# Kernel optimization log

Hardware: AMD Instinct MI355X
Metric: run time of the kernel (lower is better)

## Reference

```python
import jax, jax.numpy as jnp
import numpy as np
from jax import lax

B, C, L = 64, 768, 197
DEG = 3          # KACN Chebyshev degree
KW = 3           # conv kernel size
EPS = 1e-5       # BatchNorm eps
END_X = 14.0     # RoPE grid width (14x14 patch grid + 1 CLS token)


def _conv1d(x, W):
    # x: (B, Cin, L), W: (Cout, Cin, K); padding=1 keeps length
    return lax.conv_general_dilated(x, W, window_strides=(1,), padding=[(1, 1)],
                                    dimension_numbers=('NCH', 'OIH', 'NCH'))


def _batchnorm(y, scale, bias):
    # training-mode BatchNorm1d: biased stats over (batch, length)
    mean = jnp.mean(y, axis=(0, 2), keepdims=True)
    var = jnp.var(y, axis=(0, 2), keepdims=True)
    return (y - mean) * lax.rsqrt(var + EPS) * scale[None, :, None] + bias[None, :, None]


def _kacn_proj(x, W, scale, bias):
    # KACNConv1DLayer (groups=1): cos(arange(deg+1) * arccos(tanh(x))) basis, conv, BN
    b, c, l = x.shape
    z = jnp.arccos(jnp.tanh(x))[:, :, None, :] * jnp.arange(DEG + 1, dtype=x.dtype)[None, None, :, None]
    z = jnp.cos(z).reshape(b, c * (DEG + 1), l)  # (B, C*(DEG+1), L), channel-major pairing
    return _batchnorm(_conv1d(z, W), scale, bias)


def _rope(t, cosang, sinang):
    # rotate consecutive channel pairs; t: (B, N, C), cos/sin: (N, C//2)
    b, n, c = t.shape
    p = t.reshape(b, n, c // 2, 2)
    a, bb = p[..., 0], p[..., 1]
    ra = a * cosang[None] - bb * sinang[None]
    rb = a * sinang[None] + bb * cosang[None]
    return jnp.stack([ra, rb], axis=-1).reshape(b, n, c)


def reference(x, Wq, Wk, Wv, bnq_s, bnq_b, bnk_s, bnk_b, bnv_s, bnv_b, gamma, freqs, norm_s, norm_b):
    q = _kacn_proj(x, Wq, bnq_s, bnq_b)
    k = _kacn_proj(x, Wk, bnk_s, bnk_b)
    v = _kacn_proj(x, Wv, bnv_s, bnv_b)
    b, c, l = v.shape
    Q = q.transpose(0, 2, 1)  # (B, L, C)
    K = k.transpose(0, 2, 1)
    # mixed 2D RoPE angles (num_heads=1): t_x, t_y over 14x14 grid
    t = jnp.arange(l - 1, dtype=x.dtype)
    tx = jnp.mod(t, END_X)
    ty = jnp.floor(t / END_X)
    ang = tx[:, None] * freqs[0][None, :] + ty[:, None] * freqs[1][None, :]  # (L-1, C//2)
    cosang, sinang = jnp.cos(ang), jnp.sin(ang)
    # token 0 (CLS) is not rotated
    Qr = jnp.concatenate([Q[:, :1], _rope(Q[:, 1:], cosang, sinang)], axis=1)
    Kr = jnp.concatenate([K[:, :1], _rope(K[:, 1:], cosang, sinang)], axis=1)
    energy = jnp.einsum('bic,bjc->bij', Qr, Kr)          # unscaled, as in the module
    att = jax.nn.softmax(energy, axis=-1)
    out = jnp.einsum('bcj,bij->bci', v, att)             # v @ att^T
    return _batchnorm(gamma[0] * x + out, norm_s, norm_b)


def setup_inputs() -> dict:
    key = jax.random.key(0)
    ks = jax.random.split(key, 5)
    std = 1.0 / (C * (DEG + 1) * KW)
    x = jax.random.normal(ks[0], (B, C, L), dtype=jnp.float32)
    Wq = jax.random.normal(ks[1], (C, C * (DEG + 1), KW), dtype=jnp.float32) * std
    Wk = jax.random.normal(ks[2], (C, C * (DEG + 1), KW), dtype=jnp.float32) * std
    Wv = jax.random.normal(ks[3], (C, C * (DEG + 1), KW), dtype=jnp.float32) * std
    ones = jnp.ones((C,), jnp.float32)
    zeros = jnp.zeros((C,), jnp.float32)
    # init_2d_freqs(dim=C, num_heads=1, theta=10, rotate=True).view(2, -1)
    mag = 1.0 / 10.0 ** (np.arange(0, C, 4)[: C // 4].astype(np.float32) / C)
    ang = float(jax.random.uniform(ks[4], ())) * 2.0 * np.pi
    fx = np.concatenate([mag * np.cos(ang), mag * np.cos(np.pi / 2 + ang)])
    fy = np.concatenate([mag * np.sin(ang), mag * np.sin(np.pi / 2 + ang)])
    freqs = jnp.asarray(np.stack([fx, fy], axis=0), dtype=jnp.float32)  # (2, C//2)
    return {"x": x, "Wq": Wq, "Wk": Wk, "Wv": Wv,
            "bnq_s": ones, "bnq_b": zeros, "bnk_s": ones, "bnk_b": zeros,
            "bnv_s": ones, "bnv_b": zeros,
            "gamma": jnp.zeros((1,), jnp.float32), "freqs": freqs,
            "norm_s": ones, "norm_b": zeros}
```

## Files before the change

### kernel.cpp

```cpp
#include <hip/hip_runtime.h>

#define CCH 768
#define LL  197
#define L199 199
#define KC  2304
#define KTOT 6912
#define MK2 1769472
#define NVALID 12736
#define NROW 12608

typedef __bf16 bf16x8 __attribute__((ext_vector_type(8)));
typedef float f32x4 __attribute__((ext_vector_type(4)));
typedef float f32x16 __attribute__((ext_vector_type(16)));

__device__ __forceinline__ unsigned short f2bf(float f) {
  unsigned int u = __float_as_uint(f);
  u += 0x7FFFu + ((u >> 16) & 1u);
  return (unsigned short)(u >> 16);
}
__device__ __forceinline__ float bf2f(unsigned short h) {
  return __uint_as_float(((unsigned int)h) << 16);
}

__global__ void bias_k(const float* __restrict__ Wq, const float* __restrict__ Wk,
                       const float* __restrict__ Wv, float* __restrict__ bias3) {
  int u = blockIdx.x * 256 + threadIdx.x;
  if (u >= 9 * 768) return;
  int proj = u / 2304, rem = u % 2304, tap = rem / 768, m = rem % 768;
  const float* W = proj == 0 ? Wq : (proj == 1 ? Wk : Wv);
  float s = 0.f;
  for (int c = 0; c < 768; ++c) s += W[((size_t)m * 3072 + c * 4) * 3 + tap];
  bias3[u] = s;
}

__global__ void pack_w3(const float* __restrict__ Wq, const float* __restrict__ Wk,
                        const float* __restrict__ Wv, unsigned short* __restrict__ Apack,
                        size_t pack1_halves) {
  int u = blockIdx.x * 256 + threadIdx.x;
  if (u >= MK2) return;
  int proj = blockIdx.y;
  const float* W = proj == 0 ? Wq : (proj == 1 ? Wk : Wv);
  unsigned short* Ahi = Apack + (size_t)proj * pack1_halves;
  unsigned short* Alo = Ahi + (size_t)768 * KTOT;
  int m = u / KC, kc = u % KC;
  int c = kc / 3, dm1 = kc % 3;
  int ci = c * 4 + dm1 + 1;
  const float* src = W + ((size_t)m * 3072 + ci) * 3;
#pragma unroll
  for (int tap = 0; tap < 3; ++tap) {
    float f = src[tap];
    unsigned short hi = f2bf(f);
    unsigned short lo = f2bf(f - bf2f(hi));
    size_t idx = (size_t)m * KTOT + tap * KC + kc;
    Ahi[idx] = hi;
    Alo[idx] = lo;
  }
}

__global__ void z_kernel(const float* __restrict__ x, unsigned short* __restrict__ Zhi,
                         unsigned short* __restrict__ Zlo) {
  __shared__ float zs[3][32][33];
  int c0 = blockIdx.x * 32, l0 = blockIdx.y * 32, b = blockIdx.z;
  int t = threadIdx.x;
#pragma unroll
  for (int s = 0; s < 4; ++s) {
    int u = t + 256 * s;
    int rc = u >> 5, cl = u & 31;
    float v = 0.f;
    if (l0 + cl < LL) v = x[((size_t)b * CCH + c0 + rc) * LL + l0 + cl];
    float t1 = tanhf(v);
    zs[0][rc][cl] = t1;
    zs[1][rc][cl] = 2.f * t1 * t1 - 1.f;
    zs[2][rc][cl] = t1 * (4.f * t1 * t1 - 3.f);
  }
  __syncthreads();
#pragma unroll
  for (int s = 0; s < 12; ++s) {
    int w = t + 256 * s;
    int rl = w / 96, cc = w % 96;
    if (l0 + rl < LL) {
      int cl2 = cc / 3, dm1 = cc % 3;
      float v = zs[dm1][cl2][rl];
      unsigned short hi = f2bf(v);
      unsigned short lo = f2bf(v - bf2f(hi));
      size_t row = (size_t)b * L199 + 1 + l0 + rl;
      Zhi[row * KC + c0 * 3 + cc] = hi;
      Zlo[row * KC + c0 * 3 + cc] = lo;
    }
  }
}

__global__ void zero_zpad(unsigned short* __restrict__ Zhi, unsigned short* __restrict__ Zlo) {
  int u = blockIdx.x * 256 + threadIdx.x;
  if (u >= 132 * KC) return;
  int rowi = u / KC, c = u % KC;
  size_t r = (rowi < 128) ? ((size_t)(rowi >> 1) * L199 + (size_t)(rowi & 1) * 198)
                          : ((size_t)NVALID + rowi - 128);
  Zhi[r * KC + c] = 0;
  Zlo[r * KC + c] = 0;
}

#define GLL(SRC, DST) \
  __builtin_amdgcn_global_load_lds( \
      (const __attribute__((address_space(1))) void*)(SRC), \
      (__attribute__((address_space(3))) void*)(DST), 16, 0, 0)

__global__ __launch_bounds__(512, 2) void conv_gemm3(const unsigned short* __restrict__ Apack,
                                                     const unsigned short* __restrict__ Zhi,
                                                     const unsigned short* __restrict__ Zlo,
                                                     const float* __restrict__ bias3,
                                                     float* __restrict__ Oqk,
                                                     float* __restrict__ Ov) {
  __shared__ unsigned short lds[2 * 4 * 8192];
  const int bid = blockIdx.x;
  const int xcd = bid & 7, loc = bid >> 3;
  const int wg = (xcd < 2) ? (xcd * 57 + loc) : (114 + (xcd - 2) * 56 + loc);
  const int n_t = wg / 9, rem = wg % 9;
  const int proj = rem / 3, m_t = rem % 3;
  const int m_blk = m_t * 256, n_blk = n_t * 256;
  const unsigned short* Ahi = Apack + (size_t)proj * 2 * 768 * KTOT;
  const unsigned short* Alo = Ahi + (size_t)768 * KTOT;
  const float* bias3p = bias3 + proj * 2304;
  float* Op = (proj == 2) ? Ov : Oqk + (size_t)proj * NROW * CCH;

  const int t = threadIdx.x;
  const int wave = t >> 6, lane = t & 63;
  const int wm = (wave >> 2) * 128, wn = (wave & 3) * 64;
  f32x16 acc[4][2] = {};

  const int lt = ((lane >> 4) & 1) * 512 + (lane >> 5) * 128 + (lane & 15) * 8;
  const int auoff = (wm >> 4) * 512 + lt;
  const int buoff = (wn >> 4) * 512 + lt;

  const int prow = lane & 15;
  const int kch = lane >> 4;
  const unsigned short* srcs[8];
  int doff[8];
#pragma unroll
  for (int j = 0; j < 8; ++j) {
    int u = (wave << 3) + j;
    int tile = u >> 4, p = u & 15;
    doff[j] = tile * 8192 + p * 512;
    int r;
    const unsigned short* g;
    int rs;
    if (tile < 2) {
      r = m_blk + p * 16 + prow;
      g = (tile == 0) ? Ahi : Alo;
      rs = KTOT;
    } else {
      r = n_blk + p * 16 + prow;
      if (r > 12737) r = 12737;
      g = (tile == 2) ? Zhi : Zlo;
      rs = KC;
    }
    srcs[j] = g + (size_t)r * rs + kch * 8;
  }

  const int NIT = KTOT / 32;
#pragma unroll
  for (int j = 0; j < 8; ++j) GLL(srcs[j], lds + doff[j]);
#pragma unroll
  for (int j = 0; j < 6; ++j) GLL(srcs[j] + 32, lds + 32768 + doff[j]);
  asm volatile("s_waitcnt vmcnt(6)\n\ts_barrier" ::: "memory");
  __builtin_amdgcn_sched_barrier(0);

  for (int i = 0; i < NIT; ++i) {
    const unsigned short* lb = lds + ((i & 1) ? 32768 : 0);
    unsigned short* othbuf = lds + ((i & 1) ? 0 : 32768);
    unsigned short* curbuf = lds + ((i & 1) ? 32768 : 0);
    const int koff_prev = 32 * (i + 1);
    const int koff_cur  = 32 * (i + 2);
    const bool stage_prev = (i < NIT - 1);
    const bool stage_cur  = (i < NIT - 2);

    bf16x8 bh[2][2], bl[2][2];
    bf16x8 ah[2], al[2];

#pragma unroll
    for (int ks = 0; ks < 2; ++ks) {
#pragma unroll
      for (int nb = 0; nb < 2; ++nb) {
        bh[nb][ks] = *(const bf16x8*)(lb + 16384 + buoff + nb * 1024 + ks * 256);
        bl[nb][ks] = *(const bf16x8*)(lb + 24576 + buoff + nb * 1024 + ks * 256);
      }
      ah[ks] = *(const bf16x8*)(lb + auoff + ks * 256);
      al[ks] = *(const bf16x8*)(lb + 8192 + auoff + ks * 256);
    }
    if (stage_prev) {
      GLL(srcs[6] + koff_prev, othbuf + doff[6]);
      GLL(srcs[7] + koff_prev, othbuf + doff[7]);
    }
    asm volatile("s_barrier\n\ts_waitcnt lgkmcnt(0)" ::: "memory");
    __builtin_amdgcn_sched_barrier(0);
    __builtin_amdgcn_s_setprio(1);
#pragma unroll
    for (int p = 0; p < 3; ++p)
#pragma unroll
      for (int ks = 0; ks < 2; ++ks)
#pragma unroll
        for (int nb = 0; nb < 2; ++nb) {
          acc[0][nb] = __builtin_amdgcn_mfma_f32_32x32x16_bf16(
              p == 2 ? al[ks] : ah[ks], p == 1 ? bl[nb][ks] : bh[nb][ks], acc[0][nb], 0, 0, 0);
        }
    __builtin_amdgcn_s_setprio(0);
    asm volatile("s_barrier" ::: "memory");
    __builtin_amdgcn_sched_barrier(0);

#define PHASEQ(Q)                                                                 \
    {                                                                             \
      _Pragma("unroll") for (int ks = 0; ks < 2; ++ks) {                          \
        ah[ks] = *(const bf16x8*)(lb + auoff + (Q) * 1024 + ks * 256);            \
        al[ks] = *(const bf16x8*)(lb + 8192 + auoff + (Q) * 1024 + ks * 256);     \
      }                                                                           \
      if (stage_cur) {                                                            \
        GLL(srcs[2 * ((Q) - 1)] + koff_cur, curbuf + doff[2 * ((Q) - 1)]);        \
        GLL(srcs[2 * ((Q) - 1) + 1] + koff_cur, curbuf + doff[2 * ((Q) - 1) + 1]);\
      }                                                                           \
      asm volatile("s_barrier\n\ts_waitcnt lgkmcnt(0)" ::: "memory");             \
      __builtin_amdgcn_sched_barrier(0);                                          \
      __builtin_amdgcn_s_setprio(1);                                              \
      _Pragma("unroll") for (int p = 0; p < 3; ++p)                               \
      _Pragma("unroll") for (int ks = 0; ks < 2; ++ks)                            \
      _Pragma("unroll") for (int nb = 0; nb < 2; ++nb) {                          \
        acc[Q][nb] = __builtin_amdgcn_mfma_f32_32x32x16_bf16(                     \
            p == 2 ? al[ks] : ah[ks], p == 1 ? bl[nb][ks] : bh[nb][ks],           \
            acc[Q][nb], 0, 0, 0);                                                 \
      }                                                                           \
      __builtin_amdgcn_s_setprio(0);                                              \
    }

    PHASEQ(1)
    asm volatile("s_barrier" ::: "memory");
    __builtin_amdgcn_sched_barrier(0);
    PHASEQ(2)
    asm volatile("s_barrier" ::: "memory");
    __builtin_amdgcn_sched_barrier(0);
    PHASEQ(3)
    if (i < NIT - 2) {
      asm volatile("s_waitcnt vmcnt(6)\n\ts_barrier" ::: "memory");
    } else if (i == NIT - 2) {
      asm volatile("s_waitcnt vmcnt(0)\n\ts_barrier" ::: "memory");
    }
    __builtin_amdgcn_sched_barrier(0);
#undef PHASEQ
  }

  int rowarr[2];
  bool val[2], v0[2], v2[2];
#pragma unroll
  for (int nb = 0; nb < 2; ++nb) {
    int n = n_blk + wn + nb * 32 + (lane & 31);
    int b = n / L199, nl = n - b * L199;
    val[nb] = (n < NVALID) && (nl < LL);
    rowarr[nb] = b * LL + nl;
    v0[nb] = (nl == 0);
    v2[nb] = (nl == 196);
  }
#pragma unroll
  for (int mb = 0; mb < 4; ++mb) {
#pragma unroll
    for (int q = 0; q < 4; ++q) {
      int m = m_blk + wm + mb * 32 + q * 8 + (lane >> 5) * 4;
      f32x4 b0 = *(const f32x4*)(bias3p + m);
      f32x4 b1 = *(const f32x4*)(bias3p + 768 + m);
      f32x4 b2 = *(const f32x4*)(bias3p + 1536 + m);
      f32x4 bs = b0 + b1 + b2;
#pragma unroll
      for (int nb = 0; nb < 2; ++nb) {
        if (val[nb]) {
          f32x4 r;
          r[0] = acc[mb][nb][q * 4 + 0];
          r[1] = acc[mb][nb][q * 4 + 1];
          r[2] = acc[mb][nb][q * 4 + 2];
          r[3] = acc[mb][nb][q * 4 + 3];
          r += bs;
          if (v0[nb]) r -= b0;
          if (v2[nb]) r -= b2;
          *(f32x4*)(Op + (size_t)rowarr[nb] * CCH + m) = r;
        }
      }
    }
  }
}

__global__ void zero_f32(float* __restrict__ p, int n) {
  int u = blockIdx.x * 256 + threadIdx.x;
  if (u < n) p[u] = 0.f;
}

__global__ void bn_stats(const float* __restrict__ Oqk, const float* __restrict__ Ov,
                         float* __restrict__ Ssum, float* __restrict__ Ssq) {
  int proj = blockIdx.z;
  int cb = blockIdx.x * 64;
  int rb = blockIdx.y;
  int t = threadIdx.x;
  int ch = cb + (t & 63);
  int phase = t >> 6;
  const float* Op = (proj == 2) ? Ov : Oqk + (size_t)proj * NROW * CCH;
  float s = 0.f, q = 0.f;
  for (int r = rb * 394 + phase; r < rb * 394 + 394; r += 4) {
    float v = Op[(size_t)r * CCH + ch];
    s += v; q += v * v;
  }
  __shared__ float rs[256], rq[256];
  rs[t] = s; rq[t] = q;
  __syncthreads();
  if (t < 64) {
    float S = rs[t] + rs[t + 64] + rs[t + 128] + rs[t + 192];
    float Q = rq[t] + rq[t + 64] + rq[t + 128] + rq[t + 192];
    atomicAdd(&Ssum[proj * CCH + cb + t], S);
    atomicAdd(&Ssq[proj * CCH + cb + t], Q);
  }
}

__global__ void bn_fin(const float* __restrict__ Ssum, const float* __restrict__ Ssq,
                       const float* __restrict__ sq, const float* __restrict__ bq,
                       const float* __restrict__ sk, const float* __restrict__ bk,
                       const float* __restrict__ sv, const float* __restrict__ bv,
                       float* __restrict__ abn) {
  int u = blockIdx.x * 256 + threadIdx.x;
  if (u >= 3 * CCH) return;
  int proj = u / CCH, ch = u % CCH;
  float mean = Ssum[u] / 12608.f;
  float var = Ssq[u] / 12608.f - mean * mean;
  const float* sc = proj == 0 ? sq : (proj == 1 ? sk : sv);
  const float* bi = proj == 0 ? bq : (proj == 1 ? bk : bv);
  float a = sc[ch] * rsqrtf(var + 1e-5f);
  abn[u * 2] = a;
  abn[u * 2 + 1] = bi[ch] - mean * a;
}

__global__ void rope_pack(const float* __restrict__ Oqk, const float* __restrict__ abn,
                          const float* __restrict__ freqs, float* __restrict__ Qr,
                          float* __restrict__ Kr) {
  size_t u = (size_t)blockIdx.x * 256 + threadIdx.x;
  if (u >= 64ull * LL * 384) return;
  int c2 = (int)(u % 384);
  int l = (int)((u / 384) % LL);
  int b = (int)(u / (384ull * LL));
  size_t rowO = ((size_t)b * LL + l) * CCH + 2 * c2;
  const float* Ok = Oqk + (size_t)NROW * CCH;
  float q0 = Oqk[rowO], q1 = Oqk[rowO + 1];
  float k0 = Ok[rowO], k1 = Ok[rowO + 1];
  float aq0 = abn[(2 * c2) * 2],                bq0 = abn[(2 * c2) * 2 + 1];
  float aq1 = abn[(2 * c2 + 1) * 2],            bq1 = abn[(2 * c2 + 1) * 2 + 1];
  float ak0 = abn[(CCH + 2 * c2) * 2],          bk0 = abn[(CCH + 2 * c2) * 2 + 1];
  float ak1 = abn[(CCH + 2 * c2 + 1) * 2],      bk1 = abn[(CCH + 2 * c2 + 1) * 2 + 1];
  q0 = q0 * aq0 + bq0; q1 = q1 * aq1 + bq1;
  k0 = k0 * ak0 + bk0; k1 = k1 * ak1 + bk1;
  if (l > 0) {
    int tt = l - 1;
    float tx = (float)(tt % 14), ty = (float)(tt / 14);
    float ang = tx * freqs[c2] + ty * freqs[384 + c2];
    float sn, cs;
    sincosf(ang, &sn, &cs);
    float r0 = q0 * cs - q1 * sn, r1 = q0 * sn + q1 * cs;
    q0 = r0; q1 = r1;
    r0 = k0 * cs - k1 * sn; r1 = k0 * sn + k1 * cs;
    k0 = r0; k1 = r1;
  }
  size_t rowT = ((size_t)b * LL + l) * CCH + 2 * c2;
  Qr[rowT] = q0; Qr[rowT + 1] = q1;
  Kr[rowT] = k0; Kr[rowT + 1] = k1;
}

__global__ void energy_k(const float* __restrict__ Qr, const float* __restrict__ Kr,
                         float* __restrict__ E) {
  __shared__ float Qs[32][33], Ks[32][33];
  int i0 = blockIdx.x * 32, j0 = blockIdx.y * 32, b = blockIdx.z;
  int t = threadIdx.x, tj = t & 31, ti = t >> 5;
  float acc[4] = {0.f, 0.f, 0.f, 0.f};
  const float* Qb = Qr + (size_t)b * LL * CCH;
  const float* Kb = Kr + (size_t)b * LL * CCH;
  for (int k0 = 0; k0 < CCH; k0 += 32) {
    __syncthreads();
#pragma unroll
    for (int s = 0; s < 4; ++s) {
      int u = t + 256 * s, r = u >> 5, cc = u & 31;
      Qs[r][cc] = (i0 + r < LL) ? Qb[(size_t)(i0 + r) * CCH + k0 + cc] : 0.f;
      Ks[r][cc] = (j0 + r < LL) ? Kb[(size_t)(j0 + r) * CCH + k0 + cc] : 0.f;
    }
    __syncthreads();
#pragma unroll
    for (int kk = 0; kk < 32; ++kk) {
      float kv = Ks[tj][kk];
#pragma unroll
      for (int q = 0; q < 4; ++q) acc[q] += Qs[ti * 4 + q][kk] * kv;
    }
  }
#pragma unroll
  for (int q = 0; q < 4; ++q) {
    int i = i0 + ti * 4 + q, j = j0 + tj;
    if (i < LL && j < LL) E[((size_t)b * LL + i) * LL + j] = acc[q];
  }
}

__global__ void softmax_k(float* __restrict__ E) {
  int row = blockIdx.x;
  int lane = threadIdx.x;
  float* Er = E + (size_t)row * LL;
  float v[4];
  float m = -3.4e38f;
#pragma unroll
  for (int q = 0; q < 4; ++q) {
    int j = lane + 64 * q;
    v[q] = (j < LL) ? Er[j] : -3.4e38f;
    m = fmaxf(m, v[q]);
  }
  for (int off = 32; off; off >>= 1) m = fmaxf(m, __shfl_down(m, off));
  m = __shfl(m, 0);
  float s = 0.f;
#pragma unroll
  for (int q = 0; q < 4; ++q) {
    int j = lane + 64 * q;
    v[q] = (j < LL) ? expf(v[q] - m) : 0.f;
    s += v[q];
  }
  for (int off = 32; off; off >>= 1) s += __shfl_down(s, off);
  s = __shfl(s, 0);
  float inv = 1.f / s;
#pragma unroll
  for (int q = 0; q < 4; ++q) {
    int j = lane + 64 * q;
    if (j < LL) Er[j] = v[q] * inv;
  }
}

__global__ void av_k(const float* __restrict__ att, const float* __restrict__ Ov,
                     const float* __restrict__ abn, float* __restrict__ OA) {
  __shared__ float As[32][33];
  __shared__ float Vs[32][64];
  int i0 = blockIdx.x * 32, c0 = blockIdx.y * 64, b = blockIdx.z;
  int t = threadIdx.x, tc = t & 63, tq = t >> 6;
  const float* attb = att + (size_t)b * LL * LL;
  float acc[8] = {};
  for (int j0 = 0; j0 < LL; j0 += 32) {
    __syncthreads();
#pragma unroll
    for (int s = 0; s < 4; ++s) {
      int u = t + 256 * s, r = u >> 5, cc = u & 31;
      As[r][cc] = (i0 + r < LL && j0 + cc < LL) ? attb[(size_t)(i0 + r) * LL + j0 + cc] : 0.f;
    }
#pragma unroll
    for (int s = 0; s < 8; ++s) {
      int u = t + 256 * s, r = u >> 6, cc = u & 63;
      Vs[r][cc] = (j0 + r < LL) ? Ov[((size_t)b * LL + j0 + r) * CCH + c0 + cc] : 0.f;
    }
    __syncthreads();
#pragma unroll
    for (int jj = 0; jj < 32; ++jj) {
      float vv = Vs[jj][tc];
#pragma unroll
      for (int q = 0; q < 8; ++q) acc[q] += As[tq * 8 + q][jj] * vv;
    }
  }
  float a = abn[(2 * CCH + c0 + tc) * 2], bb = abn[(2 * CCH + c0 + tc) * 2 + 1];
#pragma unroll
  for (int q = 0; q < 8; ++q) {
    int i = i0 + tq * 8 + q;
    if (i < LL) OA[((size_t)b * LL + i) * CCH + c0 + tc] = a * acc[q] + bb;
  }
}

__global__ void trans_y(const float* __restrict__ OA, const float* __restrict__ x,
                        const float* __restrict__ gamma, float* __restrict__ Y) {
  __shared__ float Ts[32][33];
  int l0 = blockIdx.x * 32, c0 = blockIdx.y * 32, b = blockIdx.z;
  int t = threadIdx.x;
  float g = gamma[0];
#pragma unroll
  for (int s = 0; s < 4; ++s) {
    int u = t + 256 * s, r = u >> 5, cc = u & 31;
    Ts[r][cc] = (l0 + r < LL) ? OA[((size_t)b * LL + l0 + r) * CCH + c0 + cc] : 0.f;
  }
  __syncthreads();
#pragma unroll
  for (int s = 0; s < 4; ++s) {
    int u = t + 256 * s, rc = u >> 5, cl = u & 31;
    if (l0 + cl < LL) {
      size_t idx = ((size_t)b * CCH + c0 + rc) * LL + l0 + cl;
      Y[idx] = g * x[idx] + Ts[cl][rc];
    }
  }
}

__global__ void bn_y(const float* __restrict__ Y, const float* __restrict__ ns,
                     const float* __restrict__ nb, float* __restrict__ fab) {
  int c = blockIdx.x;
  int t = threadIdx.x;
  float s = 0.f, q = 0.f;
  for (int u = t; u < 12608; u += 256) {
    int b = u / LL, l = u % LL;
    float v = Y[((size_t)b * CCH + c) * LL + l];
    s += v; q += v * v;
  }
  __shared__ float rs[256], rq[256];
  rs[t] = s; rq[t] = q;
  __syncthreads();
  for (int off = 128; off; off >>= 1) {
    if (t < off) { rs[t] += rs[t + off]; rq[t] += rq[t + off]; }
    __syncthreads();
  }
  if (t == 0) {
    float mean = rs[0] / 12608.f, var = rq[0] / 12608.f - mean * mean;
    float a = ns[c] * rsqrtf(var + 1e-5f);
    fab[c * 2] = a;
    fab[c * 2 + 1] = nb[c] - mean * a;
  }
}

__global__ void final_k(const float* __restrict__ Y, const float* __restrict__ fab,
                        float* __restrict__ out) {
  size_t u = (size_t)blockIdx.x * 256 + threadIdx.x;
  if (u >= 64ull * CCH * LL) return;
  int c = (int)((u / LL) % CCH);
  out[u] = fab[c * 2] * Y[u] + fab[c * 2 + 1];
}

extern "C" void kernel_launch(void* const* d_in, const int* in_sizes, int n_in,
                              void* d_out, int out_size, void* d_ws, size_t ws_size,
                              hipStream_t stream) {
  const float* x = (const float*)d_in[0];
  const float* Wq = (const float*)d_in[1];
  const float* Wk = (const float*)d_in[2];
  const float* Wv = (const float*)d_in[3];
  const float* bnq_s = (const float*)d_in[4];
  const float* bnq_b = (const float*)d_in[5];
  const float* bnk_s = (const float*)d_in[6];
  const float* bnk_b = (const float*)d_in[7];
  const float* bnv_s = (const float*)d_in[8];
  const float* bnv_b = (const float*)d_in[9];
  const float* gamma = (const float*)d_in[10];
  const float* freqs = (const float*)d_in[11];
  const float* norm_s = (const float*)d_in[12];
  const float* norm_b = (const float*)d_in[13];
  float* out = (float*)d_out;

  char* ws = (char*)d_ws;
  const size_t QRSZ  = 38731776;
  const size_t PACK1 = 21233664;
  const size_t ZSZ   = 58705920;

  const size_t OFS_PACK = 0;
  const size_t OFS_Z    = 3 * PACK1;
  const size_t OFS_ZLO  = OFS_Z + ZSZ;
  const size_t OFS_O    = OFS_ZLO + ZSZ;
  const size_t OFS_MISC = OFS_O + 2 * QRSZ;

  unsigned short* Apack = (unsigned short*)(ws + OFS_PACK);
  unsigned short* Zhi = (unsigned short*)(ws + OFS_Z);
  unsigned short* Zlo = (unsigned short*)(ws + OFS_ZLO);
  float* Oqk = (float*)(ws + OFS_O);
  float* bias3 = (float*)(ws + OFS_MISC);
  float* Ssum = (float*)(ws + OFS_MISC + 27648);
  float* Ssq  = (float*)(ws + OFS_MISC + 36864);
  float* abn  = (float*)(ws + OFS_MISC + 46080);
  float* fab  = (float*)(ws + OFS_MISC + 64512);
  float* Ov = out;
  float* Qr = (float*)(ws + OFS_Z);
  float* Kr = (float*)(ws + OFS_Z + QRSZ);
  float* E  = (float*)(ws + OFS_Z + 2 * QRSZ);
  float* OA = (float*)(ws + OFS_Z);
  float* Y  = (float*)(ws + OFS_Z + QRSZ);

  bias_k<<<dim3(27), 256, 0, stream>>>(Wq, Wk, Wv, bias3);
  zero_zpad<<<dim3((132 * KC + 255) / 256), 256, 0, stream>>>(Zhi, Zlo);
  z_kernel<<<dim3(24, 7, 64), 256, 0, stream>>>(x, Zhi, Zlo);
  pack_w3<<<dim3((MK2 + 255) / 256, 3), 256, 0, stream>>>(Wq, Wk, Wv, Apack, PACK1 / 2);
  conv_gemm3<<<dim3(450), 512, 0, stream>>>(Apack, Zhi, Zlo, bias3, Oqk, Ov);

  zero_f32<<<dim3(18), 256, 0, stream>>>(Ssum, 4608);
  bn_stats<<<dim3(12, 32, 3), 256, 0, stream>>>(Oqk, Ov, Ssum, Ssq);
  bn_fin<<<dim3(9), 256, 0, stream>>>(Ssum, Ssq, bnq_s, bnq_b, bnk_s, bnk_b, bnv_s, bnv_b, abn);
  rope_pack<<<dim3((unsigned)((64ull * LL * 384 + 255) / 256)), 256, 0, stream>>>(Oqk, abn, freqs, Qr, Kr);
  energy_k<<<dim3(7, 7, 64), 256, 0, stream>>>(Qr, Kr, E);
  softmax_k<<<dim3(64 * LL), 64, 0, stream>>>(E);
  av_k<<<dim3(7, 12, 64), 256, 0, stream>>>(E, Ov, abn, OA);
  trans_y<<<dim3(7, 24, 64), 256, 0, stream>>>(OA, x, gamma, Y);
  bn_y<<<dim3(CCH), 256, 0, stream>>>(Y, norm_s, norm_b, fab);
  final_k<<<dim3((unsigned)((64ull * CCH * LL + 255) / 256)), 256, 0, stream>>>(Y, fab, out);
}
```

Measured before the change: 2.031 ms.

## Parallelize bias reduction across wavefronts and vectorize LDS reads in attention kernels

The bias kernel now gives each output element a full 64-lane wavefront that reduces with shuffles, replacing one serial 768-long loop per thread spread over only 27 blocks. The energy and attention-value kernels pad and transpose their shared tiles so the inner loops read with float4 and float2 vector LDS loads, cutting LDS instruction count. The transposed V store may add bank conflicts on the write side, and the changed summation order alters floating-point rounding slightly.

```diff
diff --git a/kernel.cpp b/kernel.cpp
--- a/kernel.cpp
+++ b/kernel.cpp
@@ -10,6 +10,7 @@
 #define NROW 12608
 
 typedef __bf16 bf16x8 __attribute__((ext_vector_type(8)));
+typedef float f32x2 __attribute__((ext_vector_type(2)));
 typedef float f32x4 __attribute__((ext_vector_type(4)));
 typedef float f32x16 __attribute__((ext_vector_type(16)));
 
@@ -24,13 +25,15 @@
 
 __global__ void bias_k(const float* __restrict__ Wq, const float* __restrict__ Wk,
                        const float* __restrict__ Wv, float* __restrict__ bias3) {
-  int u = blockIdx.x * 256 + threadIdx.x;
-  if (u >= 9 * 768) return;
-  int proj = u / 2304, rem = u % 2304, tap = rem / 768, m = rem % 768;
+  int w = (blockIdx.x * 256 + threadIdx.x) >> 6;
+  int lane = threadIdx.x & 63;
+  if (w >= 9 * 768) return;
+  int proj = w / 2304, rem = w % 2304, tap = rem / 768, m = rem % 768;
   const float* W = proj == 0 ? Wq : (proj == 1 ? Wk : Wv);
   float s = 0.f;
-  for (int c = 0; c < 768; ++c) s += W[((size_t)m * 3072 + c * 4) * 3 + tap];
-  bias3[u] = s;
+  for (int c = lane; c < 768; c += 64) s += W[((size_t)m * 3072 + c * 4) * 3 + tap];
+  for (int off = 32; off; off >>= 1) s += __shfl_down(s, off);
+  if (lane == 0) bias3[w] = s;
 }
 
 __global__ void pack_w3(const float* __restrict__ Wq, const float* __restrict__ Wk,
@@ -367,7 +370,7 @@
 
 __global__ void energy_k(const float* __restrict__ Qr, const float* __restrict__ Kr,
                          float* __restrict__ E) {
-  __shared__ float Qs[32][33], Ks[32][33];
+  __shared__ float Qs[32][36], Ks[32][36];
   int i0 = blockIdx.x * 32, j0 = blockIdx.y * 32, b = blockIdx.z;
   int t = threadIdx.x, tj = t & 31, ti = t >> 5;
   float acc[4] = {0.f, 0.f, 0.f, 0.f};
@@ -383,10 +386,13 @@
     }
     __syncthreads();
 #pragma unroll
-    for (int kk = 0; kk < 32; ++kk) {
-      float kv = Ks[tj][kk];
-#pragma unroll
-      for (int q = 0; q < 4; ++q) acc[q] += Qs[ti * 4 + q][kk] * kv;
+    for (int kk = 0; kk < 32; kk += 4) {
+      f32x4 kv = *(const f32x4*)&Ks[tj][kk];
+#pragma unroll
+      for (int q = 0; q < 4; ++q) {
+        f32x4 qv = *(const f32x4*)&Qs[ti * 4 + q][kk];
+        acc[q] += qv[0] * kv[0] + qv[1] * kv[1] + qv[2] * kv[2] + qv[3] * kv[3];
+      }
     }
   }
 #pragma unroll
@@ -429,8 +435,8 @@
 
 __global__ void av_k(const float* __restrict__ att, const float* __restrict__ Ov,
                      const float* __restrict__ abn, float* __restrict__ OA) {
-  __shared__ float As[32][33];
-  __shared__ float Vs[32][64];
+  __shared__ float As[32][34];
+  __shared__ float Vst[64][34];
   int i0 = blockIdx.x * 32, c0 = blockIdx.y * 64, b = blockIdx.z;
   int t = threadIdx.x, tc = t & 63, tq = t >> 6;
   const float* attb = att + (size_t)b * LL * LL;
@@ -445,14 +451,17 @@
 #pragma unroll
     for (int s = 0; s < 8; ++s) {
       int u = t + 256 * s, r = u >> 6, cc = u & 63;
-      Vs[r][cc] = (j0 + r < LL) ? Ov[((size_t)b * LL + j0 + r) * CCH + c0 + cc] : 0.f;
+      Vst[cc][r] = (j0 + r < LL) ? Ov[((size_t)b * LL + j0 + r) * CCH + c0 + cc] : 0.f;
     }
     __syncthreads();
 #pragma unroll
-    for (int jj = 0; jj < 32; ++jj) {
-      float vv = Vs[jj][tc];
-#pragma unroll
-      for (int q = 0; q < 8; ++q) acc[q] += As[tq * 8 + q][jj] * vv;
+    for (int jj = 0; jj < 32; jj += 2) {
+      f32x2 vv = *(const f32x2*)&Vst[tc][jj];
+#pragma unroll
+      for (int q = 0; q < 8; ++q) {
+        f32x2 av = *(const f32x2*)&As[tq * 8 + q][jj];
+        acc[q] += av[0] * vv[0] + av[1] * vv[1];
+      }
     }
   }
   float a = abn[(2 * CCH + c0 + tc) * 2], bb = abn[(2 * CCH + c0 + tc) * 2 + 1];
@@ -564,7 +573,7 @@
   float* OA = (float*)(ws + OFS_Z);
   float* Y  = (float*)(ws + OFS_Z + QRSZ);
 
-  bias_k<<<dim3(27), 256, 0, stream>>>(Wq, Wk, Wv, bias3);
+  bias_k<<<dim3(1728), 256, 0, stream>>>(Wq, Wk, Wv, bias3);
   zero_zpad<<<dim3((132 * KC + 255) / 256), 256, 0, stream>>>(Zhi, Zlo);
   z_kernel<<<dim3(24, 7, 64), 256, 0, stream>>>(x, Zhi, Zlo);
   pack_w3<<<dim3((MK2 + 255) / 256, 3), 256, 0, stream>>>(Wq, Wk, Wv, Apack, PACK1 / 2);
```

Measured after the change: 2.549 ms. 25.5% more time.
